# Kernel tuning notes

Hardware: AMD Instinct MI355X
Metric: run time of the kernel (lower is better)

The kernel has to match this reference:

```python
import jax, jax.numpy as jnp
import numpy as np

B, S, NI, NQK, NV = 8, 2048, 1024, 128, 128

def setup_inputs() -> dict:
    key = jax.random.key(0)
    ks = jax.random.split(key, 7)
    sc_i = 1.0 / np.sqrt(NI)
    x = jax.random.normal(ks[0], (B, S, NI), dtype=jnp.float32)
    Wq = jax.random.uniform(ks[1], (NQK, NI), dtype=jnp.float32, minval=-sc_i, maxval=sc_i)
    bq = jax.random.uniform(ks[2], (NQK,), dtype=jnp.float32, minval=-sc_i, maxval=sc_i)
    Wk = jax.random.uniform(ks[3], (NQK, NI), dtype=jnp.float32, minval=-sc_i, maxval=sc_i)
    bk = jax.random.uniform(ks[4], (NQK,), dtype=jnp.float32, minval=-sc_i, maxval=sc_i)
    Wv = jax.random.uniform(ks[5], (NV, NI), dtype=jnp.float32, minval=-sc_i, maxval=sc_i)
    bv = jax.random.uniform(ks[6], (NV,), dtype=jnp.float32, minval=-sc_i, maxval=sc_i)
    return {"x": x, "Wq": Wq, "bq": bq, "Wk": Wk, "bk": bk, "Wv": Wv, "bv": bv}

def reference(x, Wq, bq, Wk, bk, Wv, bv):
    # torch nn.Linear: y = x @ W.T + b
    q = jnp.einsum('bsi,di->bsd', x, Wq) + bq  # [B,S,NQK]
    k = jnp.einsum('bsi,di->bsd', x, Wk) + bk  # [B,S,NQK]
    v = jnp.einsum('bsi,di->bsd', x, Wv) + bv  # [B,S,NV]
    # NOTE: original has no 1/sqrt(d) scaling
    Z = jnp.einsum('bqd,bkd->bqk', q, k)       # [B,S,S]
    Z = jax.nn.softmax(Z, axis=2)
    y = jnp.einsum('bqk,bkd->bqd', Z, v)       # [B,S,NV]
    return y
```

## Files before the change

kernel.cpp:

```cpp
#include <hip/hip_runtime.h>
#include <hip/hip_bf16.h>
#include <cstdint>

#define B_ 8
#define S_ 2048
#define NI_ 1024
#define D_ 128
#define M_ (B_ * S_)

typedef __attribute__((ext_vector_type(8))) short bf16x8;
typedef __attribute__((ext_vector_type(8))) unsigned short u16x8;
typedef __attribute__((ext_vector_type(4))) float f32x4;

__device__ __forceinline__ unsigned short f2bf(float f) {
    union { float f; uint32_t u; } v; v.f = f;
    uint32_t u = v.u;
    u += 0x7fff + ((u >> 16) & 1);
    return (unsigned short)(u >> 16);
}

__global__ __launch_bounds__(256) void k_cvt_x(const float* __restrict__ x,
                                               unsigned short* __restrict__ xb) {
    int t = blockIdx.x * 256 + threadIdx.x;
    long base = (long)t * 8;
    float4 a = *(const float4*)(x + base);
    float4 b = *(const float4*)(x + base + 4);
    u16x8 r;
    r[0] = f2bf(a.x); r[1] = f2bf(a.y); r[2] = f2bf(a.z); r[3] = f2bf(a.w);
    r[4] = f2bf(b.x); r[5] = f2bf(b.y); r[6] = f2bf(b.z); r[7] = f2bf(b.w);
    *(u16x8*)(xb + base) = r;
}

__global__ __launch_bounds__(256) void k_pack_w(const float* __restrict__ Wq, const float* __restrict__ bq,
                                                const float* __restrict__ Wk, const float* __restrict__ bk,
                                                const float* __restrict__ Wv, const float* __restrict__ bv,
                                                unsigned short* __restrict__ wb, float* __restrict__ bias) {
    int t = blockIdx.x * 256 + threadIdx.x;
    int e = t * 8;
    const float* src; int off;
    if (e < 131072)      { src = Wq; off = e; }
    else if (e < 262144) { src = Wk; off = e - 131072; }
    else                 { src = Wv; off = e - 262144; }
    float4 a = *(const float4*)(src + off);
    float4 b = *(const float4*)(src + off + 4);
    u16x8 r;
    r[0] = f2bf(a.x); r[1] = f2bf(a.y); r[2] = f2bf(a.z); r[3] = f2bf(a.w);
    r[4] = f2bf(b.x); r[5] = f2bf(b.y); r[6] = f2bf(b.z); r[7] = f2bf(b.w);
    *(u16x8*)(wb + e) = r;
    if (t < 384)
        bias[t] = (t < 128) ? bq[t] : (t < 256) ? bk[t - 128] : bv[t - 256];
}

__global__ __launch_bounds__(256) void k_qkv(const unsigned short* __restrict__ xb,
                                             const unsigned short* __restrict__ wb,
                                             const float* __restrict__ bias,
                                             unsigned short* __restrict__ q,
                                             unsigned short* __restrict__ kout,
                                             unsigned short* __restrict__ vT) {
    __shared__ __align__(16) unsigned short As[128 * 32];
    __shared__ __align__(16) unsigned short Bs[128 * 32];
    const int tid = threadIdx.x;
    const int m0 = blockIdx.x * 128;
    const int n0 = blockIdx.y * 128;
    const int l = tid & 63, w = tid >> 6;
    const int wr = w >> 1, wc = w & 1;
    const int lr = l & 15, lg = l >> 4;
    const int sr = tid >> 2;
    const int sc = (tid & 3) * 8;

    f32x4 acc[4][4] = {};

    for (int k0 = 0; k0 < NI_; k0 += 32) {
        *(u16x8*)(As + sr * 32 + sc)        = *(const u16x8*)(xb + (long)(m0 + sr) * NI_ + k0 + sc);
        *(u16x8*)(As + (sr + 64) * 32 + sc) = *(const u16x8*)(xb + (long)(m0 + sr + 64) * NI_ + k0 + sc);
        *(u16x8*)(Bs + sr * 32 + sc)        = *(const u16x8*)(wb + (long)(n0 + sr) * NI_ + k0 + sc);
        *(u16x8*)(Bs + (sr + 64) * 32 + sc) = *(const u16x8*)(wb + (long)(n0 + sr + 64) * NI_ + k0 + sc);
        __syncthreads();
        bf16x8 a[4], b[4];
#pragma unroll
        for (int i = 0; i < 4; i++)
            a[i] = *(const bf16x8*)(As + (wr * 64 + i * 16 + lr) * 32 + lg * 8);
#pragma unroll
        for (int j = 0; j < 4; j++)
            b[j] = *(const bf16x8*)(Bs + (wc * 64 + j * 16 + lr) * 32 + lg * 8);
#pragma unroll
        for (int i = 0; i < 4; i++)
#pragma unroll
            for (int j = 0; j < 4; j++)
                acc[i][j] = __builtin_amdgcn_mfma_f32_16x16x32_bf16(a[i], b[j], acc[i][j], 0, 0, 0);
        __syncthreads();
    }

#pragma unroll
    for (int i = 0; i < 4; i++)
#pragma unroll
        for (int j = 0; j < 4; j++)
#pragma unroll
            for (int r = 0; r < 4; r++) {
                int row = m0 + wr * 64 + i * 16 + lg * 4 + r;
                int n = n0 + wc * 64 + j * 16 + lr;
                float val = acc[i][j][r] + bias[n];
                unsigned short bv16 = f2bf(val);
                if (n0 == 0)        q[(long)row * 128 + n] = bv16;
                else if (n0 == 128) kout[(long)row * 128 + (n - 128)] = bv16;
                else {
                    int bb = row >> 11, s = row & 2047, d = n - 256;
                    vT[((long)bb * 128 + d) * (long)S_ + s] = bv16;
                }
            }
}

#define SHIFT_ 16.0f
__global__ __launch_bounds__(256, 2) void k_attn(const unsigned short* __restrict__ q,
                                                 const unsigned short* __restrict__ kk,
                                                 const unsigned short* __restrict__ vT,
                                                 float* __restrict__ o_part,
                                                 float* __restrict__ L_part) {
    __shared__ __align__(16) unsigned short Kl[2 * 64 * 128];
    __shared__ __align__(16) unsigned short Vl[2 * 128 * 64];
    __shared__ __align__(16) unsigned short Plds[4 * 32 * 64];
    const int tid = threadIdx.x, l = tid & 63, w = tid >> 6;
    const int b = blockIdx.z, ks = blockIdx.y;
    const int q0 = blockIdx.x * 128 + w * 32;
    const int lr = l & 15, lg = l >> 4;
    const unsigned short* qB = q  + (long)b * S_ * 128;
    const unsigned short* kB = kk + (long)b * S_ * 128;
    const unsigned short* vB = vT + (long)b * 128 * S_;
    char* Pw = (char*)Plds + w * 4096;
    const int kv_base = ks * 512;
    const int lsw = (lr & 7) << 4;

    const int krow = tid >> 2, kcb = (tid & 3) * 64;
    const int vrow = tid >> 1, vcb = (tid & 1) * 64;
    const int kswz = (krow & 7) << 4, vswz = (vrow & 7) << 4;

    bf16x8 qf[2][4];
#pragma unroll
    for (int a = 0; a < 2; a++)
#pragma unroll
        for (int kc = 0; kc < 4; kc++)
            qf[a][kc] = *(const bf16x8*)(qB + (long)(q0 + a * 16 + lr) * 128 + kc * 32 + lg * 8);

    {
        const unsigned short* kg = kB + (long)(kv_base + krow) * 128 + (tid & 3) * 32;
        const unsigned short* vg = vB + (long)vrow * S_ + kv_base + (tid & 1) * 32;
        u16x8 k0v = *(const u16x8*)(kg),      k1v = *(const u16x8*)(kg + 8);
        u16x8 k2v = *(const u16x8*)(kg + 16), k3v = *(const u16x8*)(kg + 24);
        u16x8 v0v = *(const u16x8*)(vg),      v1v = *(const u16x8*)(vg + 8);
        u16x8 v2v = *(const u16x8*)(vg + 16), v3v = *(const u16x8*)(vg + 24);
        char* kd = (char*)Kl; char* vd = (char*)Vl;
        *(u16x8*)(kd + ((krow * 256 + kcb)      ^ kswz)) = k0v;
        *(u16x8*)(kd + ((krow * 256 + kcb + 16) ^ kswz)) = k1v;
        *(u16x8*)(kd + ((krow * 256 + kcb + 32) ^ kswz)) = k2v;
        *(u16x8*)(kd + ((krow * 256 + kcb + 48) ^ kswz)) = k3v;
        *(u16x8*)(vd + ((vrow * 128 + vcb)      ^ vswz)) = v0v;
        *(u16x8*)(vd + ((vrow * 128 + vcb + 16) ^ vswz)) = v1v;
        *(u16x8*)(vd + ((vrow * 128 + vcb + 32) ^ vswz)) = v2v;
        *(u16x8*)(vd + ((vrow * 128 + vcb + 48) ^ vswz)) = v3v;
    }
    __syncthreads();

    float psum[2][4] = {};
    f32x4 o[2][8] = {};
    int cur = 0;

    for (int t = 0; t < 8; t++) {
        u16x8 k0v, k1v, k2v, k3v, v0v, v1v, v2v, v3v;
        if (t < 7) {
            int kv = kv_base + (t + 1) * 64;
            const unsigned short* kg = kB + (long)(kv + krow) * 128 + (tid & 3) * 32;
            const unsigned short* vg = vB + (long)vrow * S_ + kv + (tid & 1) * 32;
            k0v = *(const u16x8*)(kg);      k1v = *(const u16x8*)(kg + 8);
            k2v = *(const u16x8*)(kg + 16); k3v = *(const u16x8*)(kg + 24);
            v0v = *(const u16x8*)(vg);      v1v = *(const u16x8*)(vg + 8);
            v2v = *(const u16x8*)(vg + 16); v3v = *(const u16x8*)(vg + 24);
        }

        const char* kd = (const char*)Kl + cur * 16384;
        const char* vd = (const char*)Vl + cur * 16384;

        f32x4 sa[2][4] = {};
#pragma unroll
        for (int j = 0; j < 4; j++) {
            bf16x8 kf[4];
#pragma unroll
            for (int kc = 0; kc < 4; kc++)
                kf[kc] = *(const bf16x8*)(kd + (((j * 16 + lr) * 256 + kc * 64 + lg * 16) ^ lsw));
#pragma unroll
            for (int a = 0; a < 2; a++)
#pragma unroll
                for (int kc = 0; kc < 4; kc++)
                    sa[a][j] = __builtin_amdgcn_mfma_f32_16x16x32_bf16(qf[a][kc], kf[kc], sa[a][j], 0, 0, 0);
        }

#pragma unroll
        for (int a = 0; a < 2; a++)
#pragma unroll
            for (int r = 0; r < 4; r++) {
                int row = a * 16 + lg * 4 + r;
#pragma unroll
                for (int j = 0; j < 4; j++) {
                    float pj = __expf(sa[a][j][r] - SHIFT_);
                    psum[a][r] += pj;
                    int bo = (row * 128 + (j * 16 + lr) * 2) ^ ((row & 7) << 4);
                    *(unsigned short*)(Pw + bo) = f2bf(pj);
                }
            }

        bf16x8 pa[2][2];
#pragma unroll
        for (int a = 0; a < 2; a++) {
            pa[a][0] = *(const bf16x8*)(Pw + (((a * 16 + lr) * 128 + lg * 16) ^ lsw));
            pa[a][1] = *(const bf16x8*)(Pw + (((a * 16 + lr) * 128 + 64 + lg * 16) ^ lsw));
        }

#pragma unroll
        for (int c = 0; c < 8; c++) {
            int dr = c * 16 + lr;
            bf16x8 vf0 = *(const bf16x8*)(vd + ((dr * 128 + lg * 16) ^ lsw));
            bf16x8 vf1 = *(const bf16x8*)(vd + ((dr * 128 + 64 + lg * 16) ^ lsw));
#pragma unroll
            for (int a = 0; a < 2; a++) {
                o[a][c] = __builtin_amdgcn_mfma_f32_16x16x32_bf16(pa[a][0], vf0, o[a][c], 0, 0, 0);
                o[a][c] = __builtin_amdgcn_mfma_f32_16x16x32_bf16(pa[a][1], vf1, o[a][c], 0, 0, 0);
            }
        }

        if (t < 7) {
            char* kdn = (char*)Kl + (cur ^ 1) * 16384;
            char* vdn = (char*)Vl + (cur ^ 1) * 16384;
            *(u16x8*)(kdn + ((krow * 256 + kcb)      ^ kswz)) = k0v;
            *(u16x8*)(kdn + ((krow * 256 + kcb + 16) ^ kswz)) = k1v;
            *(u16x8*)(kdn + ((krow * 256 + kcb + 32) ^ kswz)) = k2v;
            *(u16x8*)(kdn + ((krow * 256 + kcb + 48) ^ kswz)) = k3v;
            *(u16x8*)(vdn + ((vrow * 128 + vcb)      ^ vswz)) = v0v;
            *(u16x8*)(vdn + ((vrow * 128 + vcb + 16) ^ vswz)) = v1v;
            *(u16x8*)(vdn + ((vrow * 128 + vcb + 32) ^ vswz)) = v2v;
            *(u16x8*)(vdn + ((vrow * 128 + vcb + 48) ^ vswz)) = v3v;
        }
        __syncthreads();
        cur ^= 1;
    }

#pragma unroll
    for (int a = 0; a < 2; a++)
#pragma unroll
        for (int r = 0; r < 4; r++) {
            float ps = psum[a][r];
            ps += __shfl_xor(ps, 1);
            ps += __shfl_xor(ps, 2);
            ps += __shfl_xor(ps, 4);
            ps += __shfl_xor(ps, 8);
            if (lr == 0)
                L_part[((long)ks * B_ + b) * S_ + q0 + a * 16 + lg * 4 + r] = ps;
        }
#pragma unroll
    for (int a = 0; a < 2; a++)
#pragma unroll
        for (int c = 0; c < 8; c++)
#pragma unroll
            for (int r = 0; r < 4; r++) {
                int row = q0 + a * 16 + lg * 4 + r, col = c * 16 + lr;
                o_part[(((long)ks * B_ + b) * S_ + row) * 128 + col] = o[a][c][r];
            }
}

__global__ __launch_bounds__(256) void k_comb(const float* __restrict__ op,
                                              const float* __restrict__ Lp,
                                              float* __restrict__ out) {
    int t = blockIdx.x * 256 + threadIdx.x;
    int row = t >> 5;
    int c4 = (t & 31) * 4;
    float ax = 0.f, ay = 0.f, az = 0.f, aw = 0.f, Ls = 0.f;
#pragma unroll
    for (int ts = 0; ts < 4; ts++) {
        float4 v = *(const float4*)(op + (((long)ts * M_ + row) << 7) + c4);
        ax += v.x; ay += v.y; az += v.z; aw += v.w;
        Ls += Lp[(long)ts * M_ + row];
    }
    float inv = 1.f / Ls;
    float4 r; r.x = ax * inv; r.y = ay * inv; r.z = az * inv; r.w = aw * inv;
    *(float4*)(out + ((long)row << 7) + c4) = r;
}

extern "C" void kernel_launch(void* const* d_in, const int* in_sizes, int n_in,
                              void* d_out, int out_size, void* d_ws, size_t ws_size,
                              hipStream_t stream) {
    const float* x  = (const float*)d_in[0];
    const float* Wq = (const float*)d_in[1];
    const float* bq = (const float*)d_in[2];
    const float* Wk = (const float*)d_in[3];
    const float* bk = (const float*)d_in[4];
    const float* Wv = (const float*)d_in[5];
    const float* bv = (const float*)d_in[6];
    float* out = (float*)d_out;

    char* ws = (char*)d_ws;
    unsigned short* xb   = (unsigned short*)(ws);
    unsigned short* wb   = (unsigned short*)(ws + 33554432);
    float*          bias = (float*)(ws + 33554432 + 786432);
    unsigned short* qb   = (unsigned short*)(ws + 34344960);
    unsigned short* kb   = (unsigned short*)(ws + 38539264);
    unsigned short* vT   = (unsigned short*)(ws + 42733568);
    float* o_part = (float*)(ws);
    float* L_part = (float*)(ws + 46927872);

    k_cvt_x<<<8192, 256, 0, stream>>>(x, xb);
    k_pack_w<<<192, 256, 0, stream>>>(Wq, bq, Wk, bk, Wv, bv, wb, bias);
    k_qkv<<<dim3(128, 3), 256, 0, stream>>>(xb, wb, bias, qb, kb, vT);
    k_attn<<<dim3(16, 4, 8), 256, 0, stream>>>(qb, kb, vT, o_part, L_part);
    k_comb<<<2048, 256, 0, stream>>>(o_part, L_part, out);
}
```

Baseline: 94.07 us.

## Use global_load_lds in QKV GEMM, single-buffer attention LDS, split KV eightfold

The QKV projection GEMM now copies tiles straight from global memory into LDS with global_load_lds instead of staging them through registers. The attention kernel drops double-buffered K/V LDS in favour of a single buffer with extra barriers and raises launch bounds to 3 blocks per CU. The KV split factor becomes a runtime parameter that is set to 8 when the workspace is large enough, doubling the grid. The intent is more parallelism and occupancy, at the cost of more partial outputs for the combine kernel, more barrier stalls, and lost load/compute overlap in attention.

```diff
diff --git a/kernel.cpp b/kernel.cpp
--- a/kernel.cpp
+++ b/kernel.cpp
@@ -17,6 +17,11 @@
     uint32_t u = v.u;
     u += 0x7fff + ((u >> 16) & 1);
     return (unsigned short)(u >> 16);
+}
+
+__device__ __forceinline__ void gload16(const void* g, void* l) {
+    __builtin_amdgcn_global_load_lds((const __attribute__((address_space(1))) void*)g,
+                                     (__attribute__((address_space(3))) void*)l, 16, 0, 0);
 }
 
 __global__ __launch_bounds__(256) void k_cvt_x(const float* __restrict__ x,
@@ -71,10 +76,10 @@
     f32x4 acc[4][4] = {};
 
     for (int k0 = 0; k0 < NI_; k0 += 32) {
-        *(u16x8*)(As + sr * 32 + sc)        = *(const u16x8*)(xb + (long)(m0 + sr) * NI_ + k0 + sc);
-        *(u16x8*)(As + (sr + 64) * 32 + sc) = *(const u16x8*)(xb + (long)(m0 + sr + 64) * NI_ + k0 + sc);
-        *(u16x8*)(Bs + sr * 32 + sc)        = *(const u16x8*)(wb + (long)(n0 + sr) * NI_ + k0 + sc);
-        *(u16x8*)(Bs + (sr + 64) * 32 + sc) = *(const u16x8*)(wb + (long)(n0 + sr + 64) * NI_ + k0 + sc);
+        gload16(xb + (long)(m0 + sr) * NI_ + k0 + sc,        As + tid * 8);
+        gload16(xb + (long)(m0 + 64 + sr) * NI_ + k0 + sc,   As + 2048 + tid * 8);
+        gload16(wb + (long)(n0 + sr) * NI_ + k0 + sc,        Bs + tid * 8);
+        gload16(wb + (long)(n0 + 64 + sr) * NI_ + k0 + sc,   Bs + 2048 + tid * 8);
         __syncthreads();
         bf16x8 a[4], b[4];
 #pragma unroll
@@ -111,13 +116,14 @@
 }
 
 #define SHIFT_ 16.0f
-__global__ __launch_bounds__(256, 2) void k_attn(const unsigned short* __restrict__ q,
+__global__ __launch_bounds__(256, 3) void k_attn(const unsigned short* __restrict__ q,
                                                  const unsigned short* __restrict__ kk,
                                                  const unsigned short* __restrict__ vT,
                                                  float* __restrict__ o_part,
-                                                 float* __restrict__ L_part) {
-    __shared__ __align__(16) unsigned short Kl[2 * 64 * 128];
-    __shared__ __align__(16) unsigned short Vl[2 * 128 * 64];
+                                                 float* __restrict__ L_part,
+                                                 int nsplit) {
+    __shared__ __align__(16) unsigned short Kl[64 * 128];
+    __shared__ __align__(16) unsigned short Vl[128 * 64];
     __shared__ __align__(16) unsigned short Plds[4 * 32 * 64];
     const int tid = threadIdx.x, l = tid & 63, w = tid >> 6;
     const int b = blockIdx.z, ks = blockIdx.y;
@@ -127,13 +133,36 @@
     const unsigned short* kB = kk + (long)b * S_ * 128;
     const unsigned short* vB = vT + (long)b * 128 * S_;
     char* Pw = (char*)Plds + w * 4096;
-    const int kv_base = ks * 512;
+    const int span = S_ / nsplit;
+    const int ntiles = span >> 6;
+    const int kv_base = ks * span;
     const int lsw = (lr & 7) << 4;
 
     const int krow = tid >> 2, kcb = (tid & 3) * 64;
     const int vrow = tid >> 1, vcb = (tid & 1) * 64;
     const int kswz = (krow & 7) << 4, vswz = (vrow & 7) << 4;
 
+    u16x8 k0v, k1v, k2v, k3v, v0v, v1v, v2v, v3v;
+
+#define LOADREGS(kvoff) do { \
+    const unsigned short* kg = kB + (long)((kvoff) + krow) * 128 + (tid & 3) * 32; \
+    const unsigned short* vg = vB + (long)vrow * S_ + (kvoff) + (tid & 1) * 32; \
+    k0v = *(const u16x8*)(kg);      k1v = *(const u16x8*)(kg + 8); \
+    k2v = *(const u16x8*)(kg + 16); k3v = *(const u16x8*)(kg + 24); \
+    v0v = *(const u16x8*)(vg);      v1v = *(const u16x8*)(vg + 8); \
+    v2v = *(const u16x8*)(vg + 16); v3v = *(const u16x8*)(vg + 24); } while (0)
+
+#define WRITELDS() do { \
+    char* kd_ = (char*)Kl; char* vd_ = (char*)Vl; \
+    *(u16x8*)(kd_ + ((krow * 256 + kcb)      ^ kswz)) = k0v; \
+    *(u16x8*)(kd_ + ((krow * 256 + kcb + 16) ^ kswz)) = k1v; \
+    *(u16x8*)(kd_ + ((krow * 256 + kcb + 32) ^ kswz)) = k2v; \
+    *(u16x8*)(kd_ + ((krow * 256 + kcb + 48) ^ kswz)) = k3v; \
+    *(u16x8*)(vd_ + ((vrow * 128 + vcb)      ^ vswz)) = v0v; \
+    *(u16x8*)(vd_ + ((vrow * 128 + vcb + 16) ^ vswz)) = v1v; \
+    *(u16x8*)(vd_ + ((vrow * 128 + vcb + 32) ^ vswz)) = v2v; \
+    *(u16x8*)(vd_ + ((vrow * 128 + vcb + 48) ^ vswz)) = v3v; } while (0)
+
     bf16x8 qf[2][4];
 #pragma unroll
     for (int a = 0; a < 2; a++)
@@ -141,43 +170,19 @@
         for (int kc = 0; kc < 4; kc++)
             qf[a][kc] = *(const bf16x8*)(qB + (long)(q0 + a * 16 + lr) * 128 + kc * 32 + lg * 8);
 
-    {
-        const unsigned short* kg = kB + (long)(kv_base + krow) * 128 + (tid & 3) * 32;
-        const unsigned short* vg = vB + (long)vrow * S_ + kv_base + (tid & 1) * 32;
-        u16x8 k0v = *(const u16x8*)(kg),      k1v = *(const u16x8*)(kg + 8);
-        u16x8 k2v = *(const u16x8*)(kg + 16), k3v = *(const u16x8*)(kg + 24);
-        u16x8 v0v = *(const u16x8*)(vg),      v1v = *(const u16x8*)(vg + 8);
-        u16x8 v2v = *(const u16x8*)(vg + 16), v3v = *(const u16x8*)(vg + 24);
-        char* kd = (char*)Kl; char* vd = (char*)Vl;
-        *(u16x8*)(kd + ((krow * 256 + kcb)      ^ kswz)) = k0v;
-        *(u16x8*)(kd + ((krow * 256 + kcb + 16) ^ kswz)) = k1v;
-        *(u16x8*)(kd + ((krow * 256 + kcb + 32) ^ kswz)) = k2v;
-        *(u16x8*)(kd + ((krow * 256 + kcb + 48) ^ kswz)) = k3v;
-        *(u16x8*)(vd + ((vrow * 128 + vcb)      ^ vswz)) = v0v;
-        *(u16x8*)(vd + ((vrow * 128 + vcb + 16) ^ vswz)) = v1v;
-        *(u16x8*)(vd + ((vrow * 128 + vcb + 32) ^ vswz)) = v2v;
-        *(u16x8*)(vd + ((vrow * 128 + vcb + 48) ^ vswz)) = v3v;
-    }
+    LOADREGS(kv_base);
+    WRITELDS();
     __syncthreads();
 
     float psum[2][4] = {};
     f32x4 o[2][8] = {};
-    int cur = 0;
-
-    for (int t = 0; t < 8; t++) {
-        u16x8 k0v, k1v, k2v, k3v, v0v, v1v, v2v, v3v;
-        if (t < 7) {
-            int kv = kv_base + (t + 1) * 64;
-            const unsigned short* kg = kB + (long)(kv + krow) * 128 + (tid & 3) * 32;
-            const unsigned short* vg = vB + (long)vrow * S_ + kv + (tid & 1) * 32;
-            k0v = *(const u16x8*)(kg);      k1v = *(const u16x8*)(kg + 8);
-            k2v = *(const u16x8*)(kg + 16); k3v = *(const u16x8*)(kg + 24);
-            v0v = *(const u16x8*)(vg);      v1v = *(const u16x8*)(vg + 8);
-            v2v = *(const u16x8*)(vg + 16); v3v = *(const u16x8*)(vg + 24);
-        }
-
-        const char* kd = (const char*)Kl + cur * 16384;
-        const char* vd = (const char*)Vl + cur * 16384;
+
+    for (int t = 0; t < ntiles; t++) {
+        bool more = (t + 1 < ntiles);
+        if (more) LOADREGS(kv_base + (t + 1) * 64);
+
+        const char* kd = (const char*)Kl;
+        const char* vd = (const char*)Vl;
 
         f32x4 sa[2][4] = {};
 #pragma unroll
@@ -226,20 +231,11 @@
             }
         }
 
-        if (t < 7) {
-            char* kdn = (char*)Kl + (cur ^ 1) * 16384;
-            char* vdn = (char*)Vl + (cur ^ 1) * 16384;
-            *(u16x8*)(kdn + ((krow * 256 + kcb)      ^ kswz)) = k0v;
-            *(u16x8*)(kdn + ((krow * 256 + kcb + 16) ^ kswz)) = k1v;
-            *(u16x8*)(kdn + ((krow * 256 + kcb + 32) ^ kswz)) = k2v;
-            *(u16x8*)(kdn + ((krow * 256 + kcb + 48) ^ kswz)) = k3v;
-            *(u16x8*)(vdn + ((vrow * 128 + vcb)      ^ vswz)) = v0v;
-            *(u16x8*)(vdn + ((vrow * 128 + vcb + 16) ^ vswz)) = v1v;
-            *(u16x8*)(vdn + ((vrow * 128 + vcb + 32) ^ vswz)) = v2v;
-            *(u16x8*)(vdn + ((vrow * 128 + vcb + 48) ^ vswz)) = v3v;
-        }
-        __syncthreads();
-        cur ^= 1;
+        if (more) {
+            __syncthreads();
+            WRITELDS();
+            __syncthreads();
+        }
     }
 
 #pragma unroll
@@ -263,17 +259,18 @@
                 int row = q0 + a * 16 + lg * 4 + r, col = c * 16 + lr;
                 o_part[(((long)ks * B_ + b) * S_ + row) * 128 + col] = o[a][c][r];
             }
+#undef LOADREGS
+#undef WRITELDS
 }
 
 __global__ __launch_bounds__(256) void k_comb(const float* __restrict__ op,
                                               const float* __restrict__ Lp,
-                                              float* __restrict__ out) {
+                                              float* __restrict__ out, int nsplit) {
     int t = blockIdx.x * 256 + threadIdx.x;
     int row = t >> 5;
     int c4 = (t & 31) * 4;
     float ax = 0.f, ay = 0.f, az = 0.f, aw = 0.f, Ls = 0.f;
-#pragma unroll
-    for (int ts = 0; ts < 4; ts++) {
+    for (int ts = 0; ts < nsplit; ts++) {
         float4 v = *(const float4*)(op + (((long)ts * M_ + row) << 7) + c4);
         ax += v.x; ay += v.y; az += v.z; aw += v.w;
         Ls += Lp[(long)ts * M_ + row];
@@ -302,12 +299,22 @@
     unsigned short* qb   = (unsigned short*)(ws + 34344960);
     unsigned short* kb   = (unsigned short*)(ws + 38539264);
     unsigned short* vT   = (unsigned short*)(ws + 42733568);
-    float* o_part = (float*)(ws);
-    float* L_part = (float*)(ws + 46927872);
+
+    const size_t NEED8 = 46927872ull + 67108864ull + 524288ull;
+    int nsplit; float *o_part, *L_part;
+    if (ws_size >= NEED8) {
+        nsplit = 8;
+        o_part = (float*)(ws + 46927872);
+        L_part = (float*)(ws + 46927872 + 67108864);
+    } else {
+        nsplit = 4;
+        o_part = (float*)(ws);
+        L_part = (float*)(ws + 46927872);
+    }
 
     k_cvt_x<<<8192, 256, 0, stream>>>(x, xb);
     k_pack_w<<<192, 256, 0, stream>>>(Wq, bq, Wk, bk, Wv, bv, wb, bias);
     k_qkv<<<dim3(128, 3), 256, 0, stream>>>(xb, wb, bias, qb, kb, vT);
-    k_attn<<<dim3(16, 4, 8), 256, 0, stream>>>(qb, kb, vT, o_part, L_part);
-    k_comb<<<2048, 256, 0, stream>>>(o_part, L_part, out);
-}
+    k_attn<<<dim3(16, nsplit, 8), 256, 0, stream>>>(qb, kb, vT, o_part, L_part, nsplit);
+    k_comb<<<2048, 256, 0, stream>>>(o_part, L_part, out, nsplit);
+}
```

Result: slower. 241.7 us (+157.0%).
